# Optimization experiments

Hardware: AMD Instinct MI355X
Metric: run time of the kernel (lower is better)

## Reference

```python
import jax, jax.numpy as jnp
import numpy as np
from jax import lax

N_HEADS = 8
D_K = 64
D_V = 64
TEMP = float(np.sqrt(D_K))  # MixtureOfSoftMax temperature = d_k ** 0.5


def avg_pool_3x3_s2_same(x):
    """TF-style AveragePooling2D(pool=3, stride=2, padding='same'), NHWC.
    TF excludes padded elements from the average (divide by valid count)."""
    sums = lax.reduce_window(x, 0.0, lax.add, (1, 3, 3, 1), (1, 2, 2, 1), 'SAME')
    ones = jnp.ones(x.shape[:3] + (1,), x.dtype)
    cnt = lax.reduce_window(ones, 0.0, lax.add, (1, 3, 3, 1), (1, 2, 2, 1), 'SAME')
    return sums / cnt


def conv1x1(x, w, b):
    # 1x1 conv == per-pixel channel matmul
    return jnp.einsum('bhwc,cd->bhwd', x, w) + b


def setup_inputs() -> dict:
    key = jax.random.key(0)
    ks = jax.random.split(key, 6)
    C = 512
    s1 = float(np.sqrt(2.0 / (C + D_K)))  # init_weight1 std
    s3 = float(np.sqrt(2.0 / (C + D_V)))  # init_weight3 std
    return {
        'x':   jax.random.normal(ks[0], (4, 64, 64, C), jnp.float32),
        'w_q': jax.random.normal(ks[1], (C, N_HEADS * D_K), jnp.float32) * s1,
        'b_q': jnp.zeros((N_HEADS * D_K,), jnp.float32),
        'w_k': jax.random.normal(ks[2], (C, N_HEADS * D_K), jnp.float32) * s1,
        'b_k': jnp.zeros((N_HEADS * D_K,), jnp.float32),
        'w_v': jax.random.normal(ks[3], (C, N_HEADS * D_V), jnp.float32) * s3,
        'b_v': jnp.zeros((N_HEADS * D_V,), jnp.float32),
        'w_o': jax.random.normal(ks[4], (N_HEADS * D_V, C), jnp.float32) * 0.02,
        'b_o': jnp.zeros((C,), jnp.float32),
    }


def reference(x, w_q, b_q, w_k, b_k, w_v, b_v, w_o, b_o):
    BS, H, W, C = x.shape
    residual = x
    # Q from full-res x; K, V from 3x3/s2 average-pooled x (pooling=True)
    qt = conv1x1(x, w_q, b_q).reshape(BS * N_HEADS, H * W, -1)          # (B*h, N, d_k)
    xp = avg_pool_3x3_s2_same(x)                                         # (BS, H/2, W/2, C)
    kt = conv1x1(xp, w_k, b_k).reshape(BS * N_HEADS, H * W // 4, -1)     # (B*h, N/4, d_k)
    vt = conv1x1(xp, w_v, b_v).reshape(BS * N_HEADS, H * W // 4, -1)     # (B*h, N/4, d_v)
    # MixtureOfSoftMaxACF with n_mix=1: scaled dot-product softmax attention
    attn = jnp.einsum('bnd,bmd->bnm', qt, kt) / TEMP                     # (B*h, N, N/4)
    attn = jax.nn.softmax(attn, axis=-1)                                 # dropout=identity (inference)
    out = jnp.einsum('bnm,bmd->bnd', attn, vt)                           # (B*h, N, d_v)
    out = out.reshape(BS, H, W, -1)
    out = conv1x1(out, w_o, b_o)                                         # conv1x1_bn_relu (Conv2D only in call)
    return out + residual                                                # concat=False -> Add
```

## Files before the change

### kernel.cpp

```cpp
#include <hip/hip_runtime.h>
#include <hip/hip_bf16.h>
#include <math.h>

typedef short bf16x8 __attribute__((ext_vector_type(8)));
typedef float f32x4 __attribute__((ext_vector_type(4)));
typedef unsigned short u16;

__device__ inline float b2f(u16 h) {
    unsigned int u = ((unsigned int)h) << 16;
    float f;
    __builtin_memcpy(&f, &u, 4);
    return f;
}

__device__ inline u16 f2b(float f) {
    unsigned int u;
    __builtin_memcpy(&u, &f, 4);
    unsigned int lsb = (u >> 16) & 1u;
    u += 0x7fffu + lsb;
    return (u16)(u >> 16);
}

__device__ __forceinline__ void gl2lds16(const u16* g, u16* l) {
    __builtin_amdgcn_global_load_lds(
        (const __attribute__((address_space(1))) unsigned int*)g,
        (__attribute__((address_space(3))) unsigned int*)l,
        16, 0, 0);
}

#define PITCH 72

#define QSCALE 0.18033688011112042f

__global__ __launch_bounds__(256) void prep_kernel(const float* __restrict__ x,
                                                   u16* __restrict__ xb,
                                                   const float* __restrict__ w0,
                                                   const float* __restrict__ w1,
                                                   const float* __restrict__ w2,
                                                   const float* __restrict__ w3,
                                                   u16* __restrict__ wt,
                                                   u16* __restrict__ xp) {
    __shared__ u16 T[64 * PITCH];
    int tid = threadIdx.x;
    if (blockIdx.x < 8192) {
        int idx = blockIdx.x * 256 + tid;
        float4 v = ((const float4*)x)[idx];
        ushort4 o;
        o.x = f2b(v.x); o.y = f2b(v.y); o.z = f2b(v.z); o.w = f2b(v.w);
        ((ushort4*)xb)[idx] = o;
        return;
    }
    if (blockIdx.x >= 8448) {
        int idx = (blockIdx.x - 8448) * 256 + tid;
        int c8 = idx & 63;
        int j = (idx >> 6) & 31;
        int i = (idx >> 11) & 31;
        int b = idx >> 16;
        int r0 = 2 * i, c0 = 2 * j;
        int rmax = min(r0 + 3, 64), cmax = min(c0 + 3, 64);
        float acc[8] = {};
        for (int r = r0; r < rmax; ++r)
            for (int cc = c0; cc < cmax; ++cc) {
                const float* p = &x[(size_t)((((b << 6) + r) << 6) + cc) * 512 + c8 * 8];
                float4 v0 = *(const float4*)p;
                float4 v1 = *(const float4*)(p + 4);
                acc[0] += v0.x; acc[1] += v0.y; acc[2] += v0.z; acc[3] += v0.w;
                acc[4] += v1.x; acc[5] += v1.y; acc[6] += v1.z; acc[7] += v1.w;
            }
        float inv = 1.f / (float)((rmax - r0) * (cmax - c0));
        u16 o[8];
#pragma unroll
        for (int t = 0; t < 8; ++t) o[t] = f2b(acc[t] * inv);
        *(int4*)(&xp[(size_t)idx * 8]) = *(int4*)o;
        return;
    }
    int t5 = blockIdx.x - 8192;
    int bx = t5 & 7, by = (t5 >> 3) & 7, bz = t5 >> 6;
    const float* W = bz == 0 ? w0 : bz == 1 ? w1 : bz == 2 ? w2 : w3;
    u16* WT = wt + (size_t)bz * 262144;
    int nB = bx * 64, kB = by * 64;
#pragma unroll
    for (int t = 0; t < 4; ++t) {
        int e = tid + t * 256;
        int r = e >> 4, c4 = (e & 15) * 4;
        float4 v = *(const float4*)(&W[(size_t)(kB + r) * 512 + nB + c4]);
        u16* dst = &T[r * PITCH + c4];
        dst[0] = f2b(v.x); dst[1] = f2b(v.y); dst[2] = f2b(v.z); dst[3] = f2b(v.w);
    }
    __syncthreads();
    int n = tid & 63, kg = tid >> 6;
#pragma unroll
    for (int p = 0; p < 2; ++p) {
        int k0 = (kg + p * 4) * 8;
        u16 tmp[8];
#pragma unroll
        for (int i = 0; i < 8; ++i) tmp[i] = T[(k0 + i) * PITCH + n];
        *(int4*)(&WT[(size_t)(nB + n) * 512 + kB + k0]) = *(int4*)tmp;
    }
}

template <int OM, int BN, int GY>
__device__ __forceinline__ void gemm_body(int bid,
                                          const u16* __restrict__ A,
                                          const u16* __restrict__ WT,
                                          const float* __restrict__ bias,
                                          const float* __restrict__ bias2res,
                                          void* __restrict__ Cv,
                                          void* __restrict__ Cv2,
                                          float oscale,
                                          u16* At, u16* Bt) {
    int tid = threadIdx.x, lane = tid & 63, wave = tid >> 6;
    int q = lane >> 4, l16 = lane & 15;
    constexpr int MI = (BN == 128) ? 2 : 1;
    int wm, wn;
    if constexpr (BN == 128) { wm = wave & 1; wn = wave >> 1; }
    else                     { wm = wave;     wn = 0; }
    int nBlk = bid / GY;
    int mBlk = bid - nBlk * GY;
    int nBase = nBlk * BN, mBase = mBlk * 64;
    f32x4 acc[MI][4] = {};

    for (int kk = 0; kk < 512; kk += 64) {
        __syncthreads();
#pragma unroll
        for (int t = 0; t < 2; ++t) {
            int c = tid + t * 256;
            int m = c >> 3, kc = (c & 7) ^ (m & 7);
            gl2lds16(&A[(size_t)(mBase + m) * 512 + kk + kc * 8], &At[c * 8]);
        }
#pragma unroll
        for (int t = 0; t < BN / 32; ++t) {
            int c = tid + t * 256;
            int m = c >> 3, kc = (c & 7) ^ (m & 7);
            gl2lds16(&WT[(size_t)(nBase + m) * 512 + kk + kc * 8], &Bt[c * 8]);
        }
        __syncthreads();
#pragma unroll
        for (int ds = 0; ds < 2; ++ds) {
            bf16x8 a[MI], b[4];
#pragma unroll
            for (int i = 0; i < MI; ++i) {
                int ma = (BN == 128 ? wm * 32 : wm * 16) + i * 16 + l16;
                a[i] = *(bf16x8*)(&At[ma * 64 + ((((ds << 2) + q) ^ (ma & 7)) << 3)]);
            }
#pragma unroll
            for (int j = 0; j < 4; ++j) {
                int nb = wn * 64 + j * 16 + l16;
                b[j] = *(bf16x8*)(&Bt[nb * 64 + ((((ds << 2) + q) ^ (nb & 7)) << 3)]);
            }
#pragma unroll
            for (int i = 0; i < MI; ++i)
#pragma unroll
                for (int j = 0; j < 4; ++j)
                    acc[i][j] = __builtin_amdgcn_mfma_f32_16x16x32_bf16(a[i], b[j], acc[i][j], 0, 0, 0);
        }
    }

    bool isK = (OM != 3) || (nBase < 512);
#pragma unroll
    for (int j = 0; j < 4; ++j) {
        int col = nBase + wn * 64 + j * 16 + l16;
        float bv;
        if constexpr (OM == 3) bv = isK ? bias[col] : bias2res[col - 512];
        else bv = bias[col];
#pragma unroll
        for (int i = 0; i < MI; ++i) {
#pragma unroll
            for (int r = 0; r < 4; ++r) {
                int row = mBase + (BN == 128 ? wm * 32 : wm * 16) + i * 16 + q * 4 + r;
                float v = acc[i][j][r] + bv;
                if constexpr (OM == 1) {
                    v += bias2res[(size_t)row * 512 + col];
                    ((float*)Cv)[(size_t)row * 512 + col] = v;
                } else if constexpr (OM == 0) {
                    ((u16*)Cv)[(size_t)row * 512 + col] = f2b(v * oscale);
                } else {
                    if (isK) {
                        ((u16*)Cv)[(size_t)row * 512 + col] = f2b(v);
                    } else {
                        int colv = col - 512;
                        int g = row >> 7, m2 = ((row & 127) << 3) + (colv >> 6), d = colv & 63;
                        ((u16*)Cv2)[(size_t)((g << 6) + d) * 1024 + m2] = f2b(v);
                    }
                }
            }
        }
    }
}

__global__ __launch_bounds__(256, 4) void qkv_kernel(const u16* __restrict__ xb,
                                                     const u16* __restrict__ xp,
                                                     const u16* __restrict__ wT,
                                                     const float* __restrict__ b_q,
                                                     const float* __restrict__ b_k,
                                                     const float* __restrict__ b_v,
                                                     u16* __restrict__ Qw,
                                                     u16* __restrict__ Kw,
                                                     u16* __restrict__ VwT) {
    __shared__ __align__(16) u16 At[64 * 64];
    __shared__ __align__(16) u16 Bt[128 * 64];
    int gid = blockIdx.x;
    if (gid < 1024) {
        gemm_body<0, 128, 256>(gid, xb, wT, b_q, nullptr, Qw, nullptr, QSCALE, At, Bt);
    } else {
        gemm_body<3, 64, 64>(gid - 1024, xp, wT + 262144, b_k, b_v, Kw, VwT, 1.0f, At, Bt);
    }
}

__global__ __launch_bounds__(256, 4) void gemm_o_kernel(const u16* __restrict__ Ow,
                                                        const u16* __restrict__ wTo,
                                                        const float* __restrict__ b_o,
                                                        const float* __restrict__ xres,
                                                        float* __restrict__ out) {
    __shared__ __align__(16) u16 At[64 * 64];
    __shared__ __align__(16) u16 Bt[128 * 64];
    gemm_body<1, 128, 256>(blockIdx.x, Ow, wTo, b_o, xres, out, nullptr, 1.0f, At, Bt);
}

__global__ __launch_bounds__(256, 4) void attn_kernel(const u16* __restrict__ Q,
                                                      const u16* __restrict__ K,
                                                      const u16* __restrict__ VT_g,
                                                      u16* __restrict__ O,
                                                      int qt0) {
    int g = blockIdx.x;
    int qtile = qt0 + blockIdx.y;
    const u16* Qg = Q + (size_t)g * 262144;
    const u16* Kg = K + (size_t)g * 65536;
    const u16* Vt = VT_g + (size_t)g * 65536;
    u16* Og = O + (size_t)g * 262144;

    __shared__ __align__(16) u16 Kt[2][64 * 64];
    __shared__ __align__(16) u16 VTs[2][64 * 64];
    __shared__ __align__(16) u16 Pt[64 * 64];

    int tid = threadIdx.x, lane = tid & 63, wave = tid >> 6;
    int q = lane >> 4, l16 = lane & 15;
    int n0 = qtile * 128;
    int pkey = (l16 & 7) << 2;
    int prow = (wave * 16 + l16) * 32;
    int* Pt32 = (int*)Pt;

    bf16x8 qf[2][2];
#pragma unroll
    for (int s = 0; s < 2; ++s)
#pragma unroll
        for (int ds = 0; ds < 2; ++ds)
            qf[s][ds] = *(const bf16x8*)(
                &Qg[(size_t)(n0 + s * 64 + wave * 16 + l16) * 64 + ds * 32 + q * 8]);

    f32x4 oacc[2][4] = {};
    float rsum[2] = {0.f, 0.f};

    auto stage = [&](int buf, int kb) {
#pragma unroll
        for (int t = 0; t < 2; ++t) {
            int c = tid + t * 256;
            int m = c >> 3, kc = (c & 7) ^ (m & 7);
            gl2lds16(&Kg[(size_t)(kb * 64 + m) * 64 + kc * 8], &Kt[buf][c * 8]);
            gl2lds16(&Vt[(size_t)m * 1024 + kb * 64 + kc * 8], &VTs[buf][c * 8]);
        }
    };

    stage(0, 0);
    asm volatile("s_waitcnt vmcnt(0)" ::: "memory");
    __syncthreads();

    int cur = 0;
#pragma unroll 1
    for (int kb = 0; kb < 16; ++kb) {
        if (kb < 15) stage(cur ^ 1, kb + 1);
        const u16* KtB = Kt[cur];
        const u16* VTsB = VTs[cur];
#pragma unroll
        for (int s = 0; s < 2; ++s) {
#pragma unroll
            for (int cb = 0; cb < 4; ++cb) {
                int m = cb * 16 + l16;
                bf16x8 kf0 = *(const bf16x8*)(&KtB[m * 64 + ((q ^ (m & 7)) << 3)]);
                bf16x8 kf1 = *(const bf16x8*)(&KtB[m * 64 + (((4 + q) ^ (m & 7)) << 3)]);
                f32x4 z = {};
                __builtin_amdgcn_s_setprio(1);
                z = __builtin_amdgcn_mfma_f32_16x16x32_bf16(kf0, qf[s][0], z, 0, 0, 0);
                z = __builtin_amdgcn_mfma_f32_16x16x32_bf16(kf1, qf[s][1], z, 0, 0, 0);
                __builtin_amdgcn_s_setprio(0);
                float p0 = __builtin_amdgcn_exp2f(z[0]);
                float p1 = __builtin_amdgcn_exp2f(z[1]);
                float p2 = __builtin_amdgcn_exp2f(z[2]);
                float p3 = __builtin_amdgcn_exp2f(z[3]);
                rsum[s] += (p0 + p1) + (p2 + p3);
                unsigned w0, w1;
                asm("v_cvt_pk_bf16_f32 %0, %1, %2" : "=v"(w0) : "v"(p0), "v"(p1));
                asm("v_cvt_pk_bf16_f32 %0, %1, %2" : "=v"(w1) : "v"(p2), "v"(p3));
                int2 w;
                w.x = (int)w0;
                w.y = (int)w1;
                int pd = (cb * 8 + q * 2) ^ pkey;
                *(int2*)(&Pt32[prow + pd]) = w;
            }
#pragma unroll
            for (int ds = 0; ds < 2; ++ds) {
                int pd = (ds * 16 + q * 4) ^ pkey;
                bf16x8 ap = *(bf16x8*)(&Pt32[prow + pd]);
                __builtin_amdgcn_s_setprio(1);
#pragma unroll
                for (int db = 0; db < 4; ++db) {
                    int dd = db * 16 + l16;
                    int jj = ds * 4 + q;
                    bf16x8 vb = *(const bf16x8*)(&VTsB[dd * 64 + ((jj ^ (dd & 7)) << 3)]);
                    oacc[s][db] = __builtin_amdgcn_mfma_f32_16x16x32_bf16(ap, vb, oacc[s][db], 0, 0, 0);
                }
                __builtin_amdgcn_s_setprio(0);
            }
        }
        asm volatile("s_waitcnt vmcnt(0)" ::: "memory");
        __syncthreads();
        cur ^= 1;
    }

#pragma unroll
    for (int s = 0; s < 2; ++s) {
        float v = rsum[s];
        v += __shfl_xor(v, 16, 64);
        v += __shfl_xor(v, 32, 64);
        rsum[s] = v;
    }
    float inv[2][4];
#pragma unroll
    for (int s = 0; s < 2; ++s)
#pragma unroll
        for (int r = 0; r < 4; ++r)
            inv[s][r] = 1.f / __shfl(rsum[s], q * 4 + r, 64);
#pragma unroll
    for (int s = 0; s < 2; ++s)
#pragma unroll
        for (int db = 0; db < 4; ++db)
#pragma unroll
            for (int r = 0; r < 4; ++r) {
                int row = n0 + s * 64 + wave * 16 + q * 4 + r;
                Og[(size_t)row * 64 + db * 16 + l16] = f2b(oacc[s][db][r] * inv[s][r]);
            }
}

extern "C" void kernel_launch(void* const* d_in, const int* in_sizes, int n_in,
                              void* d_out, int out_size, void* d_ws, size_t ws_size,
                              hipStream_t stream) {
    const float* x   = (const float*)d_in[0];
    const float* w_q = (const float*)d_in[1];
    const float* b_q = (const float*)d_in[2];
    const float* w_k = (const float*)d_in[3];
    const float* b_k = (const float*)d_in[4];
    const float* w_v = (const float*)d_in[5];
    const float* b_v = (const float*)d_in[6];
    const float* w_o = (const float*)d_in[7];
    const float* b_o = (const float*)d_in[8];
    float* out = (float*)d_out;

    char* ws = (char*)d_ws;
    u16* xb  = (u16*)(ws);
    u16* xp  = (u16*)(ws + (16ull << 20));
    u16* Qw  = (u16*)(ws + (20ull << 20));
    u16* Kw  = (u16*)(ws + (36ull << 20));
    u16* VwT = (u16*)(ws + (40ull << 20));
    u16* wT  = (u16*)(ws + (44ull << 20));
    u16* Ow  = xb;

    prep_kernel<<<9472, 256, 0, stream>>>(x, xb, w_q, w_k, w_v, w_o, wT, xp);
    qkv_kernel<<<2048, 256, 0, stream>>>(xb, xp, wT, b_q, b_k, b_v, Qw, Kw, VwT);
    attn_kernel<<<dim3(32, 16), 256, 0, stream>>>(Qw, Kw, VwT, Ow, 0);
    attn_kernel<<<dim3(32, 16), 256, 0, stream>>>(Qw, Kw, VwT, Ow, 16);
    gemm_o_kernel<<<1024, 256, 0, stream>>>(Ow, wT + 786432, b_o, x, out);
}
```

Measured before the change: 214.9 us.

## Fuse fp32-to-bf16 conversion of x into the Q GEMM tile load

Drops the separate pass that converts the full x tensor to bf16 in the prep kernel. The Q projection GEMM now loads fp32 tiles of x directly into a doubled LDS buffer and converts them to bf16 with packed convert instructions before the MFMA. The two attention launches are also merged into a single launch over all query tiles. This removes a full read/write pass over x, at the cost of double the LDS traffic for the A tile and extra convert instructions inside the GEMM inner loop.

Result: faster. 194.5 us (-9.5%).

```diff
diff --git a/kernel.cpp b/kernel.cpp
--- a/kernel.cpp
+++ b/kernel.cpp
@@ -33,7 +33,6 @@
 #define QSCALE 0.18033688011112042f
 
 __global__ __launch_bounds__(256) void prep_kernel(const float* __restrict__ x,
-                                                   u16* __restrict__ xb,
                                                    const float* __restrict__ w0,
                                                    const float* __restrict__ w1,
                                                    const float* __restrict__ w2,
@@ -42,16 +41,8 @@
                                                    u16* __restrict__ xp) {
     __shared__ u16 T[64 * PITCH];
     int tid = threadIdx.x;
-    if (blockIdx.x < 8192) {
-        int idx = blockIdx.x * 256 + tid;
-        float4 v = ((const float4*)x)[idx];
-        ushort4 o;
-        o.x = f2b(v.x); o.y = f2b(v.y); o.z = f2b(v.z); o.w = f2b(v.w);
-        ((ushort4*)xb)[idx] = o;
-        return;
-    }
-    if (blockIdx.x >= 8448) {
-        int idx = (blockIdx.x - 8448) * 256 + tid;
+    if (blockIdx.x >= 256) {
+        int idx = (blockIdx.x - 256) * 256 + tid;
         int c8 = idx & 63;
         int j = (idx >> 6) & 31;
         int i = (idx >> 11) & 31;
@@ -74,7 +65,7 @@
         *(int4*)(&xp[(size_t)idx * 8]) = *(int4*)o;
         return;
     }
-    int t5 = blockIdx.x - 8192;
+    int t5 = blockIdx.x;
     int bx = t5 & 7, by = (t5 >> 3) & 7, bz = t5 >> 6;
     const float* W = bz == 0 ? w0 : bz == 1 ? w1 : bz == 2 ? w2 : w3;
     u16* WT = wt + (size_t)bz * 262144;
@@ -99,9 +90,9 @@
     }
 }
 
-template <int OM, int BN, int GY>
+template <int OM, int BN, int GY, bool AF32>
 __device__ __forceinline__ void gemm_body(int bid,
-                                          const u16* __restrict__ A,
+                                          const void* __restrict__ Av,
                                           const u16* __restrict__ WT,
                                           const float* __restrict__ bias,
                                           const float* __restrict__ bias2res,
@@ -122,11 +113,23 @@
 
     for (int kk = 0; kk < 512; kk += 64) {
         __syncthreads();
-#pragma unroll
-        for (int t = 0; t < 2; ++t) {
-            int c = tid + t * 256;
-            int m = c >> 3, kc = (c & 7) ^ (m & 7);
-            gl2lds16(&A[(size_t)(mBase + m) * 512 + kk + kc * 8], &At[c * 8]);
+        if constexpr (AF32) {
+            const float* Af = (const float*)Av;
+#pragma unroll
+            for (int t = 0; t < 4; ++t) {
+                int c = tid + t * 256;
+                int m = c >> 4, kc = (c & 15) ^ (m & 15);
+                gl2lds16((const u16*)&Af[(size_t)(mBase + m) * 512 + kk + kc * 4],
+                         &At[c * 8]);
+            }
+        } else {
+            const u16* Ab = (const u16*)Av;
+#pragma unroll
+            for (int t = 0; t < 2; ++t) {
+                int c = tid + t * 256;
+                int m = c >> 3, kc = (c & 7) ^ (m & 7);
+                gl2lds16(&Ab[(size_t)(mBase + m) * 512 + kk + kc * 8], &At[c * 8]);
+            }
         }
 #pragma unroll
         for (int t = 0; t < BN / 32; ++t) {
@@ -141,7 +144,23 @@
 #pragma unroll
             for (int i = 0; i < MI; ++i) {
                 int ma = (BN == 128 ? wm * 32 : wm * 16) + i * 16 + l16;
-                a[i] = *(bf16x8*)(&At[ma * 64 + ((((ds << 2) + q) ^ (ma & 7)) << 3)]);
+                if constexpr (AF32) {
+                    const float* Ar = (const float*)At + ma * 64;
+                    int c0 = ((ds << 3) + (q << 1)) ^ (ma & 15);
+                    int c1 = c0 ^ 1;
+                    float4 v0 = *(const float4*)(Ar + c0 * 4);
+                    float4 v1 = *(const float4*)(Ar + c1 * 4);
+                    unsigned r0, r1, r2, r3;
+                    asm("v_cvt_pk_bf16_f32 %0, %1, %2" : "=v"(r0) : "v"(v0.x), "v"(v0.y));
+                    asm("v_cvt_pk_bf16_f32 %0, %1, %2" : "=v"(r1) : "v"(v0.z), "v"(v0.w));
+                    asm("v_cvt_pk_bf16_f32 %0, %1, %2" : "=v"(r2) : "v"(v1.x), "v"(v1.y));
+                    asm("v_cvt_pk_bf16_f32 %0, %1, %2" : "=v"(r3) : "v"(v1.z), "v"(v1.w));
+                    int4 tmp;
+                    tmp.x = (int)r0; tmp.y = (int)r1; tmp.z = (int)r2; tmp.w = (int)r3;
+                    __builtin_memcpy(&a[i], &tmp, 16);
+                } else {
+                    a[i] = *(bf16x8*)(&At[ma * 64 + ((((ds << 2) + q) ^ (ma & 7)) << 3)]);
+                }
             }
 #pragma unroll
             for (int j = 0; j < 4; ++j) {
@@ -188,7 +207,7 @@
     }
 }
 
-__global__ __launch_bounds__(256, 4) void qkv_kernel(const u16* __restrict__ xb,
+__global__ __launch_bounds__(256, 4) void qkv_kernel(const float* __restrict__ x,
                                                      const u16* __restrict__ xp,
                                                      const u16* __restrict__ wT,
                                                      const float* __restrict__ b_q,
@@ -197,13 +216,13 @@
                                                      u16* __restrict__ Qw,
                                                      u16* __restrict__ Kw,
                                                      u16* __restrict__ VwT) {
-    __shared__ __align__(16) u16 At[64 * 64];
+    __shared__ __align__(16) u16 At[64 * 128];
     __shared__ __align__(16) u16 Bt[128 * 64];
     int gid = blockIdx.x;
     if (gid < 1024) {
-        gemm_body<0, 128, 256>(gid, xb, wT, b_q, nullptr, Qw, nullptr, QSCALE, At, Bt);
+        gemm_body<0, 128, 256, true>(gid, x, wT, b_q, nullptr, Qw, nullptr, QSCALE, At, Bt);
     } else {
-        gemm_body<3, 64, 64>(gid - 1024, xp, wT + 262144, b_k, b_v, Kw, VwT, 1.0f, At, Bt);
+        gemm_body<3, 64, 64, false>(gid - 1024, xp, wT + 262144, b_k, b_v, Kw, VwT, 1.0f, At, Bt);
     }
 }
 
@@ -214,16 +233,15 @@
                                                         float* __restrict__ out) {
     __shared__ __align__(16) u16 At[64 * 64];
     __shared__ __align__(16) u16 Bt[128 * 64];
-    gemm_body<1, 128, 256>(blockIdx.x, Ow, wTo, b_o, xres, out, nullptr, 1.0f, At, Bt);
+    gemm_body<1, 128, 256, false>(blockIdx.x, Ow, wTo, b_o, xres, out, nullptr, 1.0f, At, Bt);
 }
 
 __global__ __launch_bounds__(256, 4) void attn_kernel(const u16* __restrict__ Q,
                                                       const u16* __restrict__ K,
                                                       const u16* __restrict__ VT_g,
-                                                      u16* __restrict__ O,
-                                                      int qt0) {
+                                                      u16* __restrict__ O) {
     int g = blockIdx.x;
-    int qtile = qt0 + blockIdx.y;
+    int qtile = blockIdx.y;
     const u16* Qg = Q + (size_t)g * 262144;
     const u16* Kg = K + (size_t)g * 65536;
     const u16* Vt = VT_g + (size_t)g * 65536;
@@ -356,17 +374,15 @@
     float* out = (float*)d_out;
 
     char* ws = (char*)d_ws;
-    u16* xb  = (u16*)(ws);
+    u16* Ow  = (u16*)(ws);
     u16* xp  = (u16*)(ws + (16ull << 20));
     u16* Qw  = (u16*)(ws + (20ull << 20));
     u16* Kw  = (u16*)(ws + (36ull << 20));
     u16* VwT = (u16*)(ws + (40ull << 20));
     u16* wT  = (u16*)(ws + (44ull << 20));
-    u16* Ow  = xb;
-
-    prep_kernel<<<9472, 256, 0, stream>>>(x, xb, w_q, w_k, w_v, w_o, wT, xp);
-    qkv_kernel<<<2048, 256, 0, stream>>>(xb, xp, wT, b_q, b_k, b_v, Qw, Kw, VwT);
-    attn_kernel<<<dim3(32, 16), 256, 0, stream>>>(Qw, Kw, VwT, Ow, 0);
-    attn_kernel<<<dim3(32, 16), 256, 0, stream>>>(Qw, Kw, VwT, Ow, 16);
+
+    prep_kernel<<<1280, 256, 0, stream>>>(x, w_q, w_k, w_v, w_o, wT, xp);
+    qkv_kernel<<<2048, 256, 0, stream>>>(x, xp, wT, b_q, b_k, b_v, Qw, Kw, VwT);
+    attn_kernel<<<dim3(32, 32), 256, 0, stream>>>(Qw, Kw, VwT, Ow);
     gemm_o_kernel<<<1024, 256, 0, stream>>>(Ow, wT + 786432, b_o, x, out);
 }
```
